# Performance work log

Hardware: AMD Instinct MI355X
Metric: run time of the kernel (lower is better)

The kernel has to match this reference:

```python
import jax, jax.numpy as jnp
import numpy as np

D_MODEL = 256
N_HEADS_SA = 8
CA_HEADS = 8
CA_DH = 64
CA_INNER = CA_HEADS * CA_DH  # 512
N_POINTS = 4
D_FFN = 1024
OFFSET_SCALE = 2.0
B, NQ = 4, 1024
T, H, W = 4, 64, 64
LV = T * H * W

PNAMES = ['sa_Wq','sa_bq','sa_Wk','sa_bk','sa_Wv','sa_bv','sa_Wo','sa_bo',
          'ln1_g','ln1_b','ln2_g','ln2_b','ln3_g','ln3_b',
          'ca_Wq','ca_bq','ca_Wk','ca_bk','ca_Wv','ca_bv','ca_Wref','ca_bref',
          'ca_Woff','ca_boff','ca_Wo','ca_bo',
          'ffn_W1','ffn_b1','ffn_W2','ffn_b2']


def _layer_norm(x, g, b, eps=1e-5):
    m = x.mean(-1, keepdims=True)
    v = ((x - m) ** 2).mean(-1, keepdims=True)
    return (x - m) * jax.lax.rsqrt(v + eps) * g + b


def _mha(q, k, v, Wq, bq, Wk, bk, Wv, bv, Wo, bo, n_heads):
    Bq, N, D = q.shape
    dh = D // n_heads
    scale = 1.0 / float(np.sqrt(dh))
    qh = (q @ Wq + bq).reshape(Bq, N, n_heads, dh)
    kh = (k @ Wk + bk).reshape(Bq, N, n_heads, dh)
    vh = (v @ Wv + bv).reshape(Bq, N, n_heads, dh)
    attn = jax.nn.softmax(jnp.einsum('bqhd,bkhd->bhqk', qh, kh) * scale, -1)
    out = jnp.einsum('bhqk,bkhd->bqhd', attn, vh).reshape(Bq, N, D)
    return out @ Wo + bo


def _trilinear_sample(vol, loc, sizes_f):
    # vol: [B, L, Hd, dh] flattened (T*H*W) volume per head
    # loc: [B, N, Hd, P, 3] normalized (t, h, w) coords in [0, 1]
    Bv, L, Hd, dh = vol.shape
    _, N, _, P, _ = loc.shape
    pos = jnp.clip(loc, 0.0, 1.0) * (sizes_f - 1.0)  # align_corners voxel coords
    p0 = jnp.floor(pos)
    frac = pos - p0
    p0i = p0.astype(jnp.int32)
    sizes_i = sizes_f.astype(jnp.int32)
    Hn, Wn = sizes_i[1], sizes_i[2]
    vol_t = vol.transpose(0, 2, 1, 3)  # [B, Hd, L, dh]
    out = jnp.zeros((Bv, Hd, N * P, dh), vol.dtype)
    for dt in (0, 1):
        for dy in (0, 1):
            for dx in (0, 1):
                c = jnp.minimum(p0i + jnp.array([dt, dy, dx], jnp.int32), sizes_i - 1)
                wt = (frac[..., 0] if dt else 1.0 - frac[..., 0]) \
                   * (frac[..., 1] if dy else 1.0 - frac[..., 1]) \
                   * (frac[..., 2] if dx else 1.0 - frac[..., 2])  # [B,N,Hd,P]
                idx = c[..., 0] * (Hn * Wn) + c[..., 1] * Wn + c[..., 2]
                idx_t = idx.transpose(0, 2, 1, 3).reshape(Bv, Hd, N * P, 1)
                g = jnp.take_along_axis(vol_t, idx_t, axis=2)  # [B,Hd,N*P,dh]
                w_t = wt.transpose(0, 2, 1, 3).reshape(Bv, Hd, N * P, 1)
                out = out + g * w_t
    return out.reshape(Bv, Hd, N, P, dh).transpose(0, 2, 1, 3, 4)  # [B,N,Hd,P,dh]


def _deform_cross_attn(query, key, value, flow_key, flow_value, spatial_shapes, p):
    Bq, N, _ = query.shape
    L = key.shape[1]
    sizes_f = spatial_shapes[0].astype(jnp.float32)  # single level (T, H, W)
    qh = (query @ p['ca_Wq'] + p['ca_bq']).reshape(Bq, N, CA_HEADS, CA_DH)
    ref = jax.nn.sigmoid(query @ p['ca_Wref'] + p['ca_bref'])  # [B,N,3]
    off = (query @ p['ca_Woff'] + p['ca_boff']).reshape(Bq, N, CA_HEADS, N_POINTS, 3)
    loc = ref[:, :, None, None, :] + off * (OFFSET_SCALE / sizes_f)
    k_vol = (key @ p['ca_Wk'] + p['ca_bk']).reshape(Bq, L, CA_HEADS, CA_DH)
    v_vol = (value @ p['ca_Wv'] + p['ca_bv']).reshape(Bq, L, CA_HEADS, CA_DH)
    fk_vol = (flow_key @ p['ca_Wk'] + p['ca_bk']).reshape(Bq, L, CA_HEADS, CA_DH)
    fv_vol = (flow_value @ p['ca_Wv'] + p['ca_bv']).reshape(Bq, L, CA_HEADS, CA_DH)
    k_s = _trilinear_sample(k_vol, loc, sizes_f)
    v_s = _trilinear_sample(v_vol, loc, sizes_f)
    fk_s = _trilinear_sample(fk_vol, loc, sizes_f)
    fv_s = _trilinear_sample(fv_vol, loc, sizes_f)
    scale = 1.0 / float(np.sqrt(CA_DH))
    logits = jnp.concatenate([
        jnp.einsum('bnhd,bnhpd->bnhp', qh, k_s),
        jnp.einsum('bnhd,bnhpd->bnhp', qh, fk_s)], -1) * scale
    attn = jax.nn.softmax(logits, -1)  # joint softmax over image+flow sampled points
    vals = jnp.concatenate([v_s, fv_s], 3)  # [B,N,Hd,2P,dh]
    out = jnp.einsum('bnhp,bnhpd->bnhd', attn, vals).reshape(Bq, N, CA_INNER)
    return out @ p['ca_Wo'] + p['ca_bo']


def _forward(query, query_pos, img, flow, pos_emb, spatial_shapes, p):
    q = query + query_pos
    sa = _mha(q, q, query, p['sa_Wq'], p['sa_bq'], p['sa_Wk'], p['sa_bk'],
              p['sa_Wv'], p['sa_bv'], p['sa_Wo'], p['sa_bo'], N_HEADS_SA)
    x = _layer_norm(query + sa, p['ln1_g'], p['ln1_b'])
    key = pos_emb + img
    flow_key = pos_emb + flow
    ca = _deform_cross_attn(x, key, img, flow_key, flow, spatial_shapes, p)
    x = _layer_norm(x + ca, p['ln2_g'], p['ln2_b'])
    ffn = jax.nn.relu(x @ p['ffn_W1'] + p['ffn_b1']) @ p['ffn_W2'] + p['ffn_b2']
    return _layer_norm(x + ffn, p['ln3_g'], p['ln3_b'])


def setup_inputs() -> dict:
    key = jax.random.key(0)
    ks = iter(jax.random.split(key, 64))
    def rn(shape, s=1.0):
        return jax.random.normal(next(ks), shape, jnp.float32) * s
    inp = {
        'query': rn((B, NQ, D_MODEL)),
        'query_pos': rn((B, NQ, D_MODEL)),
        'img_embed_flatten': rn((B, LV, D_MODEL)),
        'flow_embed_flatten': rn((B, LV, D_MODEL)),
        'indicator_temporal_lvl_pos_embed_flatten': rn((B, LV, D_MODEL)),
        'spatial_shapes': jnp.array([[T, H, W]], jnp.int32),
    }
    for nm in ['sa_Wq', 'sa_Wk', 'sa_Wv', 'sa_Wo']:
        inp[nm] = rn((D_MODEL, D_MODEL), 0.02)
    for nm in ['sa_bq', 'sa_bk', 'sa_bv', 'sa_bo', 'ln1_b', 'ln2_b', 'ln3_b']:
        inp[nm] = jnp.zeros((D_MODEL,), jnp.float32)
    for nm in ['ln1_g', 'ln2_g', 'ln3_g']:
        inp[nm] = jnp.ones((D_MODEL,), jnp.float32)
    inp['ca_Wq'] = rn((D_MODEL, CA_INNER), 0.02); inp['ca_bq'] = jnp.zeros((CA_INNER,), jnp.float32)
    inp['ca_Wk'] = rn((D_MODEL, CA_INNER), 0.02); inp['ca_bk'] = jnp.zeros((CA_INNER,), jnp.float32)
    inp['ca_Wv'] = rn((D_MODEL, CA_INNER), 0.02); inp['ca_bv'] = jnp.zeros((CA_INNER,), jnp.float32)
    inp['ca_Wref'] = rn((D_MODEL, 3), 0.02); inp['ca_bref'] = jnp.zeros((3,), jnp.float32)
    inp['ca_Woff'] = rn((D_MODEL, CA_HEADS * N_POINTS * 3), 0.02)
    inp['ca_boff'] = jnp.zeros((CA_HEADS * N_POINTS * 3,), jnp.float32)
    inp['ca_Wo'] = rn((CA_INNER, D_MODEL), 0.02); inp['ca_bo'] = jnp.zeros((D_MODEL,), jnp.float32)
    inp['ffn_W1'] = rn((D_MODEL, D_FFN), 0.02); inp['ffn_b1'] = jnp.zeros((D_FFN,), jnp.float32)
    inp['ffn_W2'] = rn((D_FFN, D_MODEL), 0.02); inp['ffn_b2'] = jnp.zeros((D_MODEL,), jnp.float32)
    return inp


def reference(query, query_pos, img_embed_flatten, flow_embed_flatten,
              indicator_temporal_lvl_pos_embed_flatten, spatial_shapes,
              sa_Wq, sa_bq, sa_Wk, sa_bk, sa_Wv, sa_bv, sa_Wo, sa_bo,
              ln1_g, ln1_b, ln2_g, ln2_b, ln3_g, ln3_b,
              ca_Wq, ca_bq, ca_Wk, ca_bk, ca_Wv, ca_bv, ca_Wref, ca_bref,
              ca_Woff, ca_boff, ca_Wo, ca_bo,
              ffn_W1, ffn_b1, ffn_W2, ffn_b2):
    p = dict(zip(PNAMES, (sa_Wq, sa_bq, sa_Wk, sa_bk, sa_Wv, sa_bv, sa_Wo, sa_bo,
                          ln1_g, ln1_b, ln2_g, ln2_b, ln3_g, ln3_b,
                          ca_Wq, ca_bq, ca_Wk, ca_bk, ca_Wv, ca_bv, ca_Wref, ca_bref,
                          ca_Woff, ca_boff, ca_Wo, ca_bo,
                          ffn_W1, ffn_b1, ffn_W2, ffn_b2)))
    return _forward(query, query_pos, img_embed_flatten, flow_embed_flatten,
                    indicator_temporal_lvl_pos_embed_flatten, spatial_shapes, p)
```

## Files before the change

### kernel.cpp

```cpp
#include <hip/hip_runtime.h>
#include <hip/hip_bf16.h>

#define BQ 4
#define NQT 1024
#define DM 256
#define HSA 8
#define DHSA 32
#define CAH 8
#define CADH 64
#define CAI 512
#define NPT 4
#define DFFN 1024
#define TT 4
#define HH 64
#define WW 64
#define LVOL 16384

using bf16 = __hip_bfloat16;
typedef __attribute__((ext_vector_type(4))) float fx4;
typedef __attribute__((ext_vector_type(8))) short s8v;
typedef __attribute__((ext_vector_type(4))) short s4v;

__device__ __forceinline__ float b2f(bf16 v) { return __bfloat162float(v); }
__device__ __forceinline__ bf16  f2b(float v) { return __float2bfloat16(v); }
__device__ __forceinline__ short f2bs(float v) {
  bf16 b = __float2bfloat16(v);
  return *reinterpret_cast<short*>(&b);
}

__device__ __forceinline__ float wave_sum64(float v) {
#pragma unroll
  for (int o = 32; o >= 1; o >>= 1) v += __shfl_xor(v, o, 64);
  return v;
}

__device__ __forceinline__ s8v pack8(float4 a, float4 b) {
  return (s8v){f2bs(a.x), f2bs(a.y), f2bs(a.z), f2bs(a.w),
               f2bs(b.x), f2bs(b.y), f2bs(b.z), f2bs(b.w)};
}

__device__ __forceinline__ void gl_lds16(const void* g, void* l) {
  __builtin_amdgcn_global_load_lds(
      (const __attribute__((address_space(1))) unsigned int*)g,
      (__attribute__((address_space(3))) unsigned int*)l, 16, 0, 0);
}

template <int KSH>
__global__ __launch_bounds__(256) void wtrans_k(const float* __restrict__ W,
                                               short* __restrict__ Wt, int N) {
  const int i = blockIdx.x * 256 + threadIdx.x;
  const int k = i & ((1 << KSH) - 1);
  const int n = i >> KSH;
  Wt[i] = f2bs(W[(size_t)k * N + n]);
}

template <int DUAL>
__global__ __launch_bounds__(256) void prep_k(const float* __restrict__ A,
                                              const float* __restrict__ B,
                                              short* __restrict__ O, int n4) {
  const int stride = gridDim.x * 256;
  for (int i = blockIdx.x * 256 + threadIdx.x; i < n4; i += stride) {
    float4 a = ((const float4*)A)[i];
    if (DUAL) {
      const float4 b = ((const float4*)B)[i];
      a.x += b.x; a.y += b.y; a.z += b.z; a.w += b.w;
    }
    ((s4v*)O)[i] = (s4v){f2bs(a.x), f2bs(a.y), f2bs(a.z), f2bs(a.w)};
  }
}

__global__ __launch_bounds__(256) void bgemm_k(
    const short* __restrict__ A, const short* __restrict__ Wt,
    const float* __restrict__ bias, bf16* __restrict__ Cout,
    int M, int N, int K) {
  __shared__ short As[2][128 * 32];
  __shared__ short Bs[2][128 * 32];
  const int tid = threadIdx.x;
  const int lane = tid & 63, w = tid >> 6;
  const int wr = w >> 1, wc = w & 1;
  const int lm = lane & 15, quad = lane >> 4;
  const int nwg = gridDim.x * gridDim.y;
  const int ib = blockIdx.y * gridDim.x + blockIdx.x;
  const int id = (ib & 7) * (nwg >> 3) + (ib >> 3);
  const int m0 = (id / gridDim.x) * 128;
  const int n0 = (id % gridDim.x) * 128;

  const int srow = lane >> 2;
  const int scol = (lane & 3) * 8;
  const size_t arow = (size_t)(m0 + w * 32 + srow);
  const size_t brow = (size_t)(n0 + w * 32 + srow);

  fx4 acc[4][4] = {};
  const int nt = K / 32;
  int cur = 0;
  {
    gl_lds16(&A[arow * K + scol], &As[0][(w * 32) * 32]);
    gl_lds16(&A[(arow + 16) * K + scol], &As[0][(w * 32 + 16) * 32]);
    gl_lds16(&Wt[brow * K + scol], &Bs[0][(w * 32) * 32]);
    gl_lds16(&Wt[(brow + 16) * K + scol], &Bs[0][(w * 32 + 16) * 32]);
  }
  __syncthreads();
  for (int t = 0; t < nt; t++) {
    if (t + 1 < nt) {
      const int k0 = (t + 1) * 32;
      gl_lds16(&A[arow * K + k0 + scol], &As[cur ^ 1][(w * 32) * 32]);
      gl_lds16(&A[(arow + 16) * K + k0 + scol], &As[cur ^ 1][(w * 32 + 16) * 32]);
      gl_lds16(&Wt[brow * K + k0 + scol], &Bs[cur ^ 1][(w * 32) * 32]);
      gl_lds16(&Wt[(brow + 16) * K + k0 + scol], &Bs[cur ^ 1][(w * 32 + 16) * 32]);
    }
    s8v af[4], bfr[4];
#pragma unroll
    for (int f = 0; f < 4; f++) {
      af[f] = *(s8v*)&As[cur][(wr * 64 + f * 16 + lm) * 32 + quad * 8];
      bfr[f] = *(s8v*)&Bs[cur][(wc * 64 + f * 16 + lm) * 32 + quad * 8];
    }
#pragma unroll
    for (int fm = 0; fm < 4; fm++)
#pragma unroll
      for (int fn = 0; fn < 4; fn++)
        acc[fm][fn] = __builtin_amdgcn_mfma_f32_16x16x32_bf16(
            af[fm], bfr[fn], acc[fm][fn], 0, 0, 0);
    __syncthreads();
    cur ^= 1;
  }
#pragma unroll
  for (int fn = 0; fn < 4; fn++) {
    const int n = n0 + wc * 64 + fn * 16 + lm;
    const float bb = bias[n];
#pragma unroll
    for (int fm = 0; fm < 4; fm++) {
      const int mbase = m0 + wr * 64 + fm * 16 + quad * 4;
#pragma unroll
      for (int r = 0; r < 4; r++)
        Cout[(size_t)(mbase + r) * N + n] = f2b(acc[fm][fn][r] + bb);
    }
  }
}

template <int DUAL, int RELU, int OUTBF>
__global__ __launch_bounds__(256) void mgemm_k(
    const float* __restrict__ A, const float* __restrict__ A2,
    const short* __restrict__ Wt, const float* __restrict__ bias,
    void* __restrict__ Cout, int M, int N, int K) {
  __shared__ short As[2][128 * 40];
  __shared__ short Bs[2][128 * 40];
  const int tid = threadIdx.x;
  const int lane = tid & 63, w = tid >> 6;
  const int wr = w >> 1, wc = w & 1;
  const int lm = lane & 15, quad = lane >> 4;
  const int nwg = gridDim.x * gridDim.y;
  const int ib = blockIdx.y * gridDim.x + blockIdx.x;
  const int id = (ib & 7) * (nwg >> 3) + (ib >> 3);
  const int m0 = (id / gridDim.x) * 128;
  const int n0 = (id % gridDim.x) * 128;

  const int am = tid >> 3, ak = (tid & 7) * 4;

  float4 pa[4], pa2[4];
  s8v pb[2];
  auto loadT = [&](int k0) {
#pragma unroll
    for (int i = 0; i < 4; i++) {
      pa[i] = *(const float4*)&A[(size_t)(m0 + am + i * 32) * K + k0 + ak];
      if (DUAL)
        pa2[i] = *(const float4*)&A2[(size_t)(m0 + am + i * 32) * K + k0 + ak];
    }
#pragma unroll
    for (int i = 0; i < 2; i++) {
      int unit = tid + i * 256;
      pb[i] = *(const s8v*)&Wt[(size_t)(n0 + (unit >> 2)) * K + k0 +
                               (unit & 3) * 8];
    }
  };
  auto stageT = [&](int buf) {
#pragma unroll
    for (int i = 0; i < 4; i++) {
      float x0 = pa[i].x, x1 = pa[i].y, x2 = pa[i].z, x3 = pa[i].w;
      if (DUAL) { x0 += pa2[i].x; x1 += pa2[i].y; x2 += pa2[i].z; x3 += pa2[i].w; }
      s4v sv = {f2bs(x0), f2bs(x1), f2bs(x2), f2bs(x3)};
      *(s4v*)&As[buf][(am + i * 32) * 40 + ak] = sv;
    }
#pragma unroll
    for (int i = 0; i < 2; i++) {
      int unit = tid + i * 256;
      *(s8v*)&Bs[buf][(unit >> 2) * 40 + (unit & 3) * 8] = pb[i];
    }
  };

  fx4 acc[4][4] = {};
  loadT(0);
  stageT(0);
  __syncthreads();
  int cur = 0;
  for (int k0 = 0; k0 < K; k0 += 32) {
    const int more = (k0 + 32 < K);
    if (more) loadT(k0 + 32);
    s8v af[4], bfr[4];
#pragma unroll
    for (int f = 0; f < 4; f++) {
      af[f] = *(s8v*)&As[cur][(wr * 64 + f * 16 + lm) * 40 + quad * 8];
      bfr[f] = *(s8v*)&Bs[cur][(wc * 64 + f * 16 + lm) * 40 + quad * 8];
    }
#pragma unroll
    for (int fm = 0; fm < 4; fm++)
#pragma unroll
      for (int fn = 0; fn < 4; fn++)
        acc[fm][fn] = __builtin_amdgcn_mfma_f32_16x16x32_bf16(
            af[fm], bfr[fn], acc[fm][fn], 0, 0, 0);
    if (more) stageT(cur ^ 1);
    __syncthreads();
    cur ^= 1;
  }
#pragma unroll
  for (int fn = 0; fn < 4; fn++) {
    const int n = n0 + wc * 64 + fn * 16 + lm;
    const float bb = bias[n];
#pragma unroll
    for (int fm = 0; fm < 4; fm++) {
      const int mbase = m0 + wr * 64 + fm * 16 + quad * 4;
#pragma unroll
      for (int r = 0; r < 4; r++) {
        float v = acc[fm][fn][r] + bb;
        if (RELU) v = fmaxf(v, 0.0f);
        const size_t off = (size_t)(mbase + r) * N + n;
        if (OUTBF)
          ((bf16*)Cout)[off] = f2b(v);
        else
          ((float*)Cout)[off] = v;
      }
    }
  }
}

__global__ __launch_bounds__(256) void sa_flash_k(
    const float* __restrict__ qh, const float* __restrict__ kh,
    const float* __restrict__ vh, float* __restrict__ op0,
    float* __restrict__ op1, float* __restrict__ mlb) {
  __shared__ short Ks[64 * 72];
  __shared__ short Vt[32 * 72];
  __shared__ short Ps[64 * 72];
  const int qt = blockIdx.x, h = blockIdx.y;
  const int b = blockIdx.z >> 1, half = blockIdx.z & 1;
  const int tid = threadIdx.x;
  const int w = tid >> 6, lane = tid & 63;
  const int lm = lane & 15, quad = lane >> 4;
  const size_t rowbase = (size_t)(b * NQT) * DM + h * DHSA;
  float* __restrict__ opart = half ? op1 : op0;
  float* __restrict__ ml = mlb + (size_t)half * (32768 * 2);

  s8v aq;
  {
    const int qrow = qt * 64 + w * 16 + lm;
    const float* qp = &qh[rowbase + (size_t)qrow * DM + quad * 8];
    const float4 q0 = *(const float4*)qp;
    const float4 q1 = *(const float4*)(qp + 4);
    const float sc = 0.17677669529663687f;
    aq = (s8v){f2bs(q0.x * sc), f2bs(q0.y * sc), f2bs(q0.z * sc), f2bs(q0.w * sc),
               f2bs(q1.x * sc), f2bs(q1.y * sc), f2bs(q1.z * sc), f2bs(q1.w * sc)};
  }

  fx4 o0 = {}, o1 = {};
  float mrun[4] = {-1e30f, -1e30f, -1e30f, -1e30f};
  float lrun[4] = {0.f, 0.f, 0.f, 0.f};
  const int jr = tid >> 2;
  const int d0 = (tid & 3) * 8;

  for (int jt = half * 8; jt < half * 8 + 8; jt++) {
    __syncthreads();
    {
      const size_t rb = rowbase + (size_t)(jt * 64 + jr) * DM + d0;
      const float4 k0 = *(const float4*)&kh[rb];
      const float4 k1 = *(const float4*)&kh[rb + 4];
      *(s8v*)&Ks[jr * 72 + d0] = pack8(k0, k1);
      const float4 v0 = *(const float4*)&vh[rb];
      const float4 v1 = *(const float4*)&vh[rb + 4];
      Vt[(d0 + 0) * 72 + jr] = f2bs(v0.x);
      Vt[(d0 + 1) * 72 + jr] = f2bs(v0.y);
      Vt[(d0 + 2) * 72 + jr] = f2bs(v0.z);
      Vt[(d0 + 3) * 72 + jr] = f2bs(v0.w);
      Vt[(d0 + 4) * 72 + jr] = f2bs(v1.x);
      Vt[(d0 + 5) * 72 + jr] = f2bs(v1.y);
      Vt[(d0 + 6) * 72 + jr] = f2bs(v1.z);
      Vt[(d0 + 7) * 72 + jr] = f2bs(v1.w);
    }
    __syncthreads();
    fx4 s[4];
    const fx4 zero = {};
#pragma unroll
    for (int nf = 0; nf < 4; nf++) {
      s8v kb = *(const s8v*)&Ks[(nf * 16 + lm) * 72 + quad * 8];
      s[nf] = __builtin_amdgcn_mfma_f32_16x16x32_bf16(aq, kb, zero, 0, 0, 0);
    }
#pragma unroll
    for (int r = 0; r < 4; r++) {
      float mx = fmaxf(fmaxf(s[0][r], s[1][r]), fmaxf(s[2][r], s[3][r]));
#pragma unroll
      for (int off = 8; off >= 1; off >>= 1)
        mx = fmaxf(mx, __shfl_xor(mx, off, 64));
      const float mnew = fmaxf(mrun[r], mx);
      const float corr = expf(mrun[r] - mnew);
      mrun[r] = mnew;
      float p0 = expf(s[0][r] - mnew);
      float p1 = expf(s[1][r] - mnew);
      float p2 = expf(s[2][r] - mnew);
      float p3 = expf(s[3][r] - mnew);
      float rs = p0 + p1 + p2 + p3;
#pragma unroll
      for (int off = 8; off >= 1; off >>= 1) rs += __shfl_xor(rs, off, 64);
      lrun[r] = lrun[r] * corr + rs;
      o0[r] *= corr;
      o1[r] *= corr;
      s[0][r] = p0; s[1][r] = p1; s[2][r] = p2; s[3][r] = p3;
    }
#pragma unroll
    for (int nf = 0; nf < 4; nf++)
#pragma unroll
      for (int r = 0; r < 4; r++)
        Ps[(w * 16 + quad * 4 + r) * 72 + nf * 16 + lm] = f2bs(s[nf][r]);
#pragma unroll
    for (int ks = 0; ks < 2; ks++) {
      s8v pf = *(const s8v*)&Ps[(w * 16 + lm) * 72 + ks * 32 + quad * 8];
      s8v vb0 = *(const s8v*)&Vt[lm * 72 + ks * 32 + quad * 8];
      s8v vb1 = *(const s8v*)&Vt[(16 + lm) * 72 + ks * 32 + quad * 8];
      o0 = __builtin_amdgcn_mfma_f32_16x16x32_bf16(pf, vb0, o0, 0, 0, 0);
      o1 = __builtin_amdgcn_mfma_f32_16x16x32_bf16(pf, vb1, o1, 0, 0, 0);
    }
  }
#pragma unroll
  for (int r = 0; r < 4; r++) {
    const int row = qt * 64 + w * 16 + quad * 4 + r;
    const size_t base = rowbase + (size_t)row * DM;
    opart[base + lm] = o0[r];
    opart[base + 16 + lm] = o1[r];
    if (lm == 0) {
      const int rowid = (b * 8 + h) * 1024 + row;
      ml[(size_t)rowid * 2] = mrun[r];
      ml[(size_t)rowid * 2 + 1] = lrun[r];
    }
  }
}

__global__ __launch_bounds__(256) void sa_merge_k(
    const float* __restrict__ op0, const float* __restrict__ op1,
    const float* __restrict__ mlb, float* __restrict__ outp) {
  const int t = blockIdx.x * 256 + threadIdx.x;
  const int d = t & 31;
  const int rowid = t >> 5;
  const int n = rowid & 1023, h = (rowid >> 10) & 7, b = rowid >> 13;
  const size_t addr = ((size_t)(b * NQT + n)) * DM + h * DHSA + d;
  const float m0 = mlb[(size_t)rowid * 2], l0 = mlb[(size_t)rowid * 2 + 1];
  const float m1 = mlb[65536 + (size_t)rowid * 2];
  const float l1 = mlb[65536 + (size_t)rowid * 2 + 1];
  const float M = fmaxf(m0, m1);
  const float w0 = expf(m0 - M), w1 = expf(m1 - M);
  const float inv = 1.0f / (l0 * w0 + l1 * w1);
  outp[addr] = (op0[addr] * w0 + op1[addr] * w1) * inv;
}

__global__ __launch_bounds__(128) void refoff_k(
    const float* __restrict__ x1, const float* __restrict__ Wref,
    const float* __restrict__ bref, const float* __restrict__ Woff,
    const float* __restrict__ boff, float* __restrict__ refb,
    float* __restrict__ offb) {
  __shared__ float xs[256];
  const int row = blockIdx.x;
  const int tid = threadIdx.x;
  xs[tid] = x1[(size_t)row * DM + tid];
  xs[tid + 128] = x1[(size_t)row * DM + tid + 128];
  __syncthreads();
  if (tid < 3) {
    float s = bref[tid];
    for (int d = 0; d < 256; d++) s = fmaf(xs[d], Wref[d * 3 + tid], s);
    refb[(size_t)row * 3 + tid] = 1.0f / (1.0f + expf(-s));
  } else if (tid < 99) {
    int o = tid - 3;
    float s = boff[o];
    for (int d = 0; d < 256; d++) s = fmaf(xs[d], Woff[d * 96 + o], s);
    offb[(size_t)row * 96 + o] = s;
  }
}

__device__ __forceinline__ void calc_corners(
    const float* __restrict__ refb, const float* __restrict__ offb, int bn,
    int h, int (&idxs)[NPT][8], float (&wts)[NPT][8]) {
  const float rt = refb[bn * 3 + 0], ry = refb[bn * 3 + 1], rx = refb[bn * 3 + 2];
  const float* ofp = &offb[(size_t)bn * 96 + h * 12];
#pragma unroll
  for (int p = 0; p < NPT; p++) {
    float lt = rt + ofp[p * 3 + 0] * 0.5f;
    float ly = ry + ofp[p * 3 + 1] * 0.03125f;
    float lx = rx + ofp[p * 3 + 2] * 0.03125f;
    float pt = fminf(fmaxf(lt, 0.f), 1.f) * (TT - 1);
    float py = fminf(fmaxf(ly, 0.f), 1.f) * (HH - 1);
    float px = fminf(fmaxf(lx, 0.f), 1.f) * (WW - 1);
    float f0t = floorf(pt), f0y = floorf(py), f0x = floorf(px);
    float frt = pt - f0t, fry = py - f0y, frx = px - f0x;
    int t0 = (int)f0t, y0 = (int)f0y, x0 = (int)f0x;
    int t1 = min(t0 + 1, TT - 1), y1 = min(y0 + 1, HH - 1), x1 = min(x0 + 1, WW - 1);
    float wt0 = 1.f - frt, wy0 = 1.f - fry, wx0 = 1.f - frx;
#pragma unroll
    for (int c = 0; c < 8; c++) {
      int dt = c >> 2, dy = (c >> 1) & 1, dx = c & 1;
      int ct = dt ? t1 : t0, cy = dy ? y1 : y0, cx = dx ? x1 : x0;
      idxs[p][c] = ct * (HH * WW) + cy * WW + cx;
      wts[p][c] = (dt ? frt : wt0) * (dy ? fry : wy0) * (dx ? frx : wx0);
    }
  }
}

__global__ __launch_bounds__(256) void ca_logits_k(
    const float* __restrict__ qh, const float* __restrict__ refb,
    const float* __restrict__ offb, const bf16* __restrict__ vol,
    float* __restrict__ logits, int slot) {
  const int wid = (blockIdx.x * blockDim.x + threadIdx.x) >> 6;
  const int lane = threadIdx.x & 63;
  const int h = wid & 7;
  const int bn = wid >> 3;
  const int b = bn >> 10;
  const float q = qh[(size_t)bn * CAI + h * CADH + lane];
  int idxs[NPT][8];
  float wts[NPT][8];
  calc_corners(refb, offb, bn, h, idxs, wts);
  const size_t volbase = (size_t)b * LVOL * CAI + h * CADH + lane;
  float* lp = logits + ((size_t)bn * CAH + h) * 8 + slot;
#pragma unroll
  for (int p = 0; p < NPT; p++) {
    float ks = 0.f;
#pragma unroll
    for (int c = 0; c < 8; c++)
      ks = fmaf(wts[p][c], b2f(vol[volbase + (size_t)idxs[p][c] * CAI]), ks);
    float li = wave_sum64(q * ks) * 0.125f;
    if (lane == p) lp[p] = li;
  }
}

__global__ __launch_bounds__(256) void ca_softmax_k(float* __restrict__ logits) {
  const int i = blockIdx.x * blockDim.x + threadIdx.x;
  float* p = logits + (size_t)i * 8;
  float v[8], m = -1e30f;
#pragma unroll
  for (int j = 0; j < 8; j++) { v[j] = p[j]; m = fmaxf(m, v[j]); }
  float s = 0.f;
#pragma unroll
  for (int j = 0; j < 8; j++) { v[j] = expf(v[j] - m); s += v[j]; }
  const float inv = 1.0f / s;
#pragma unroll
  for (int j = 0; j < 8; j++) p[j] = v[j] * inv;
}

template <int FIRST>
__global__ __launch_bounds__(256) void ca_acc_k(
    const float* __restrict__ refb, const float* __restrict__ offb,
    const bf16* __restrict__ vol, const float* __restrict__ attn,
    float* __restrict__ acc, int slot) {
  const int wid = (blockIdx.x * blockDim.x + threadIdx.x) >> 6;
  const int lane = threadIdx.x & 63;
  const int h = wid & 7;
  const int bn = wid >> 3;
  const int b = bn >> 10;
  int idxs[NPT][8];
  float wts[NPT][8];
  calc_corners(refb, offb, bn, h, idxs, wts);
  const size_t volbase = (size_t)b * LVOL * CAI + h * CADH + lane;
  const float* ap = attn + ((size_t)bn * CAH + h) * 8 + slot;
  const size_t off = (size_t)bn * CAI + h * CADH + lane;
  float a = FIRST ? 0.f : acc[off];
#pragma unroll
  for (int p = 0; p < NPT; p++) {
    float vs = 0.f;
#pragma unroll
    for (int c = 0; c < 8; c++)
      vs = fmaf(wts[p][c], b2f(vol[volbase + (size_t)idxs[p][c] * CAI]), vs);
    a = fmaf(ap[p], vs, a);
  }
  acc[off] = a;
}

__global__ __launch_bounds__(256) void ln_k(
    const float* __restrict__ resv, const float* __restrict__ x,
    const float* __restrict__ g, const float* __restrict__ bb,
    float* __restrict__ of) {
  const int row = (blockIdx.x * blockDim.x + threadIdx.x) >> 6;
  const int lane = threadIdx.x & 63;
  const size_t base = (size_t)row * DM;
  float v[4];
#pragma unroll
  for (int i = 0; i < 4; i++) {
    int d = lane + i * 64;
    v[i] = resv[base + d] + x[base + d];
  }
  float s = wave_sum64(v[0] + v[1] + v[2] + v[3]);
  const float mean = s * (1.0f / 256.0f);
  float vs = 0.f;
#pragma unroll
  for (int i = 0; i < 4; i++) { float d0 = v[i] - mean; vs = fmaf(d0, d0, vs); }
  vs = wave_sum64(vs);
  const float rstd = rsqrtf(vs * (1.0f / 256.0f) + 1e-5f);
#pragma unroll
  for (int i = 0; i < 4; i++) {
    int d = lane + i * 64;
    of[base + d] = (v[i] - mean) * rstd * g[d] + bb[d];
  }
}

extern "C" void kernel_launch(void* const* d_in, const int* in_sizes, int n_in,
                              void* d_out, int out_size, void* d_ws,
                              size_t ws_size, hipStream_t stream) {
  const float* query = (const float*)d_in[0];
  const float* qpos = (const float*)d_in[1];
  const float* img = (const float*)d_in[2];
  const float* flow = (const float*)d_in[3];
  const float* pos = (const float*)d_in[4];
  const float* sa_Wq = (const float*)d_in[6];
  const float* sa_Wk = (const float*)d_in[7];
  const float* sa_Wv = (const float*)d_in[8];
  const float* sa_Wo = (const float*)d_in[9];
  const float* sa_bq = (const float*)d_in[10];
  const float* sa_bk = (const float*)d_in[11];
  const float* sa_bv = (const float*)d_in[12];
  const float* sa_bo = (const float*)d_in[13];
  const float* ln1_b = (const float*)d_in[14];
  const float* ln2_b = (const float*)d_in[15];
  const float* ln3_b = (const float*)d_in[16];
  const float* ln1_g = (const float*)d_in[17];
  const float* ln2_g = (const float*)d_in[18];
  const float* ln3_g = (const float*)d_in[19];
  const float* ca_Wq = (const float*)d_in[20];
  const float* ca_bq = (const float*)d_in[21];
  const float* ca_Wk = (const float*)d_in[22];
  const float* ca_bk = (const float*)d_in[23];
  const float* ca_Wv = (const float*)d_in[24];
  const float* ca_bv = (const float*)d_in[25];
  const float* ca_Wref = (const float*)d_in[26];
  const float* ca_bref = (const float*)d_in[27];
  const float* ca_Woff = (const float*)d_in[28];
  const float* ca_boff = (const float*)d_in[29];
  const float* ca_Wo = (const float*)d_in[30];
  const float* ca_bo = (const float*)d_in[31];
  const float* ffn_W1 = (const float*)d_in[32];
  const float* ffn_b1 = (const float*)d_in[33];
  const float* ffn_W2 = (const float*)d_in[34];
  const float* ffn_b2 = (const float*)d_in[35];

  const int MQ = BQ * NQT;
  const int MV = BQ * LVOL;
  const size_t MB = 1024 * 1024;

  char* r0 = (char*)d_ws;
  char* w = r0 + 64 * MB;
  auto alloc = [&](size_t n) {
    char* p = w;
    w += (n + 255) & ~(size_t)255;
    return p;
  };
  float* x1_f = (float*)alloc((size_t)MQ * DM * 4);
  float* ca_qh = (float*)alloc((size_t)MQ * CAI * 4);
  float* refb = (float*)alloc((size_t)MQ * 3 * 4);
  float* offb = (float*)alloc((size_t)MQ * 96 * 4);
  float* logits = (float*)alloc((size_t)MQ * CAH * 8 * 4);
  float* ca_acc = (float*)alloc((size_t)MQ * CAI * 4);
  short* WtsaQ = (short*)alloc((size_t)DM * DM * 2);
  short* WtsaK = (short*)alloc((size_t)DM * DM * 2);
  short* WtsaV = (short*)alloc((size_t)DM * DM * 2);
  short* WtsaO = (short*)alloc((size_t)DM * DM * 2);
  short* Wtcaq = (short*)alloc((size_t)CAI * DM * 2);
  short* Wtk = (short*)alloc((size_t)CAI * DM * 2);
  short* Wtv = (short*)alloc((size_t)CAI * DM * 2);
  short* Wtcao = (short*)alloc((size_t)DM * CAI * 2);
  short* Wtf1 = (short*)alloc((size_t)DFFN * DM * 2);
  short* Wtf2 = (short*)alloc((size_t)DM * DFFN * 2);
  short* abuf = (short*)alloc((size_t)MV * DM * 2);
  if ((size_t)(w - (char*)d_ws) > ws_size) return;

  float* qh_sa = (float*)(r0 + 0 * MB);
  float* kh_sa = (float*)(r0 + 4 * MB);
  float* vh_sa = (float*)(r0 + 8 * MB);
  float* sa_att = (float*)(r0 + 12 * MB);
  float* sa_proj = (float*)(r0 + 16 * MB);
  float* o_p0 = (float*)(r0 + 20 * MB);
  float* o_p1 = (float*)(r0 + 24 * MB);
  float* mlb = (float*)(r0 + 28 * MB);
  bf16* vol = (bf16*)r0;
  float* ca_o = (float*)(r0 + 0 * MB);
  float* x2_f = (float*)(r0 + 4 * MB);
  float* ffn_h = (float*)(r0 + 8 * MB);
  float* ffn_o = (float*)(r0 + 24 * MB);

  const int n4v = MV * DM / 4;

  dim3 blk(256);
  wtrans_k<8><<<dim3(DM * DM / 256), blk, 0, stream>>>(sa_Wq, WtsaQ, DM);
  wtrans_k<8><<<dim3(DM * DM / 256), blk, 0, stream>>>(sa_Wk, WtsaK, DM);
  wtrans_k<8><<<dim3(DM * DM / 256), blk, 0, stream>>>(sa_Wv, WtsaV, DM);
  wtrans_k<8><<<dim3(DM * DM / 256), blk, 0, stream>>>(sa_Wo, WtsaO, DM);
  wtrans_k<8><<<dim3(DM * CAI / 256), blk, 0, stream>>>(ca_Wq, Wtcaq, CAI);
  wtrans_k<8><<<dim3(DM * CAI / 256), blk, 0, stream>>>(ca_Wk, Wtk, CAI);
  wtrans_k<8><<<dim3(DM * CAI / 256), blk, 0, stream>>>(ca_Wv, Wtv, CAI);
  wtrans_k<8><<<dim3(DM * DFFN / 256), blk, 0, stream>>>(ffn_W1, Wtf1, DFFN);
  wtrans_k<9><<<dim3(CAI * DM / 256), blk, 0, stream>>>(ca_Wo, Wtcao, DM);
  wtrans_k<10><<<dim3(DFFN * DM / 256), blk, 0, stream>>>(ffn_W2, Wtf2, DM);
  mgemm_k<1, 0, 0><<<dim3(DM / 128, MQ / 128), blk, 0, stream>>>(query, qpos, WtsaQ, sa_bq, (void*)qh_sa, MQ, DM, DM);
  mgemm_k<1, 0, 0><<<dim3(DM / 128, MQ / 128), blk, 0, stream>>>(query, qpos, WtsaK, sa_bk, (void*)kh_sa, MQ, DM, DM);
  mgemm_k<0, 0, 0><<<dim3(DM / 128, MQ / 128), blk, 0, stream>>>(query, query, WtsaV, sa_bv, (void*)vh_sa, MQ, DM, DM);
  sa_flash_k<<<dim3(16, 8, 8), blk, 0, stream>>>(qh_sa, kh_sa, vh_sa, o_p0, o_p1, mlb);
  sa_merge_k<<<dim3(4096), blk, 0, stream>>>(o_p0, o_p1, mlb, sa_att);
  mgemm_k<0, 0, 0><<<dim3(DM / 128, MQ / 128), blk, 0, stream>>>(sa_att, sa_att, WtsaO, sa_bo, (void*)sa_proj, MQ, DM, DM);
  ln_k<<<dim3(MQ / 4), blk, 0, stream>>>(query, sa_proj, ln1_g, ln1_b, x1_f);
  mgemm_k<0, 0, 0><<<dim3(CAI / 128, MQ / 128), blk, 0, stream>>>(x1_f, x1_f, Wtcaq, ca_bq, (void*)ca_qh, MQ, CAI, DM);
  refoff_k<<<dim3(MQ), dim3(128), 0, stream>>>(x1_f, ca_Wref, ca_bref, ca_Woff, ca_boff, refb, offb);
  prep_k<1><<<dim3(2048), blk, 0, stream>>>(pos, img, abuf, n4v);
  bgemm_k<<<dim3(CAI / 128, MV / 128), blk, 0, stream>>>(abuf, Wtk, ca_bk, vol, MV, CAI, DM);
  ca_logits_k<<<dim3(8192), blk, 0, stream>>>(ca_qh, refb, offb, vol, logits, 0);
  prep_k<1><<<dim3(2048), blk, 0, stream>>>(pos, flow, abuf, n4v);
  bgemm_k<<<dim3(CAI / 128, MV / 128), blk, 0, stream>>>(abuf, Wtk, ca_bk, vol, MV, CAI, DM);
  ca_logits_k<<<dim3(8192), blk, 0, stream>>>(ca_qh, refb, offb, vol, logits, 4);
  ca_softmax_k<<<dim3(128), blk, 0, stream>>>(logits);
  prep_k<0><<<dim3(2048), blk, 0, stream>>>(img, img, abuf, n4v);
  bgemm_k<<<dim3(CAI / 128, MV / 128), blk, 0, stream>>>(abuf, Wtv, ca_bv, vol, MV, CAI, DM);
  ca_acc_k<1><<<dim3(8192), blk, 0, stream>>>(refb, offb, vol, logits, ca_acc, 0);
  prep_k<0><<<dim3(2048), blk, 0, stream>>>(flow, flow, abuf, n4v);
  bgemm_k<<<dim3(CAI / 128, MV / 128), blk, 0, stream>>>(abuf, Wtv, ca_bv, vol, MV, CAI, DM);
  ca_acc_k<0><<<dim3(8192), blk, 0, stream>>>(refb, offb, vol, logits, ca_acc, 4);
  mgemm_k<0, 0, 0><<<dim3(DM / 128, MQ / 128), blk, 0, stream>>>(ca_acc, ca_acc, Wtcao, ca_bo, (void*)ca_o, MQ, DM, CAI);
  ln_k<<<dim3(MQ / 4), blk, 0, stream>>>(x1_f, ca_o, ln2_g, ln2_b, x2_f);
  mgemm_k<0, 1, 0><<<dim3(DFFN / 128, MQ / 128), blk, 0, stream>>>(x2_f, x2_f, Wtf1, ffn_b1, (void*)ffn_h, MQ, DFFN, DM);
  mgemm_k<0, 0, 0><<<dim3(DM / 128, MQ / 128), blk, 0, stream>>>(ffn_h, ffn_h, Wtf2, ffn_b2, (void*)ffn_o, MQ, DM, DFFN);
  ln_k<<<dim3(MQ / 4), blk, 0, stream>>>(x2_f, ffn_o, ln3_g, ln3_b, (float*)d_out);
}
```

Measured before the change: 728.5 us.

## Fuse fp32-to-bf16 prep into volume GEMMs, batch weight transposes, use 64-tile GEMMs

The separate prep kernels that summed or converted the fp32 volume inputs into a bf16 staging buffer are removed. The volume GEMM now loads fp32 A tiles into registers, adds and converts them, and stores them to LDS, which saves a full write and read of the 16K x 256 staging buffer for each of four passes. The ten weight-transpose launches are merged into one kernel, and the small query-side GEMMs switch to a 64x64 tile kernel so they launch more workgroups. The cost is register-staged A loads in place of direct global-to-LDS loads, plus smaller tiles with less reuse per block.

```diff
diff --git a/kernel.cpp b/kernel.cpp
--- a/kernel.cpp
+++ b/kernel.cpp
@@ -45,35 +45,30 @@
       (__attribute__((address_space(3))) unsigned int*)l, 16, 0, 0);
 }
 
-template <int KSH>
-__global__ __launch_bounds__(256) void wtrans_k(const float* __restrict__ W,
-                                               short* __restrict__ Wt, int N) {
-  const int i = blockIdx.x * 256 + threadIdx.x;
-  const int k = i & ((1 << KSH) - 1);
-  const int n = i >> KSH;
-  Wt[i] = f2bs(W[(size_t)k * N + n]);
+struct WtransArgs {
+  const float* W[10];
+  short* Wt[10];
+};
+__global__ __launch_bounds__(256) void wtrans_all_k(WtransArgs a) {
+  const int blk = blockIdx.x;
+  int seg, start, ksh, N;
+  if (blk < 1024)      { seg = blk >> 8; start = seg << 8; ksh = 8; N = 256; }
+  else if (blk < 2560) { seg = 4 + ((blk - 1024) >> 9); start = 1024 + ((seg - 4) << 9); ksh = 8; N = 512; }
+  else if (blk < 3584) { seg = 7; start = 2560; ksh = 8; N = 1024; }
+  else if (blk < 4096) { seg = 8; start = 3584; ksh = 9; N = 256; }
+  else                 { seg = 9; start = 4096; ksh = 10; N = 256; }
+  const int i = (blk - start) * 256 + threadIdx.x;
+  const int k = i & ((1 << ksh) - 1);
+  const int n = i >> ksh;
+  a.Wt[seg][i] = f2bs(a.W[seg][(size_t)k * N + n]);
 }
 
 template <int DUAL>
-__global__ __launch_bounds__(256) void prep_k(const float* __restrict__ A,
-                                              const float* __restrict__ B,
-                                              short* __restrict__ O, int n4) {
-  const int stride = gridDim.x * 256;
-  for (int i = blockIdx.x * 256 + threadIdx.x; i < n4; i += stride) {
-    float4 a = ((const float4*)A)[i];
-    if (DUAL) {
-      const float4 b = ((const float4*)B)[i];
-      a.x += b.x; a.y += b.y; a.z += b.z; a.w += b.w;
-    }
-    ((s4v*)O)[i] = (s4v){f2bs(a.x), f2bs(a.y), f2bs(a.z), f2bs(a.w)};
-  }
-}
-
-__global__ __launch_bounds__(256) void bgemm_k(
-    const short* __restrict__ A, const short* __restrict__ Wt,
-    const float* __restrict__ bias, bf16* __restrict__ Cout,
-    int M, int N, int K) {
-  __shared__ short As[2][128 * 32];
+__global__ __launch_bounds__(256) void vgemm_k(
+    const float* __restrict__ A, const float* __restrict__ A2,
+    const short* __restrict__ Wt, const float* __restrict__ bias,
+    bf16* __restrict__ Cout, int M, int N, int K) {
+  __shared__ short As[2][128 * 40];
   __shared__ short Bs[2][128 * 32];
   const int tid = threadIdx.x;
   const int lane = tid & 63, w = tid >> 6;
@@ -85,33 +80,49 @@
   const int m0 = (id / gridDim.x) * 128;
   const int n0 = (id % gridDim.x) * 128;
 
-  const int srow = lane >> 2;
-  const int scol = (lane & 3) * 8;
-  const size_t arow = (size_t)(m0 + w * 32 + srow);
-  const size_t brow = (size_t)(n0 + w * 32 + srow);
+  const int am = tid >> 3, ak = (tid & 7) * 4;
+  const size_t brow = (size_t)(n0 + w * 32 + (lane >> 2));
+  const int bcol = (lane & 3) * 8;
+
+  float4 pa[4], pa2[4];
+  auto loadA = [&](int k0) {
+#pragma unroll
+    for (int i = 0; i < 4; i++) {
+      pa[i] = *(const float4*)&A[(size_t)(m0 + am + i * 32) * K + k0 + ak];
+      if (DUAL)
+        pa2[i] = *(const float4*)&A2[(size_t)(m0 + am + i * 32) * K + k0 + ak];
+    }
+  };
+  auto glB = [&](int k0, int buf) {
+    gl_lds16(&Wt[brow * K + k0 + bcol], &Bs[buf][(w * 32) * 32]);
+    gl_lds16(&Wt[(brow + 16) * K + k0 + bcol], &Bs[buf][(w * 32 + 16) * 32]);
+  };
+  auto stageA = [&](int buf) {
+#pragma unroll
+    for (int i = 0; i < 4; i++) {
+      float x0 = pa[i].x, x1 = pa[i].y, x2 = pa[i].z, x3 = pa[i].w;
+      if (DUAL) { x0 += pa2[i].x; x1 += pa2[i].y; x2 += pa2[i].z; x3 += pa2[i].w; }
+      *(s4v*)&As[buf][(am + i * 32) * 40 + ak] =
+          (s4v){f2bs(x0), f2bs(x1), f2bs(x2), f2bs(x3)};
+    }
+  };
 
   fx4 acc[4][4] = {};
-  const int nt = K / 32;
+  loadA(0);
+  glB(0, 0);
+  stageA(0);
+  __syncthreads();
   int cur = 0;
-  {
-    gl_lds16(&A[arow * K + scol], &As[0][(w * 32) * 32]);
-    gl_lds16(&A[(arow + 16) * K + scol], &As[0][(w * 32 + 16) * 32]);
-    gl_lds16(&Wt[brow * K + scol], &Bs[0][(w * 32) * 32]);
-    gl_lds16(&Wt[(brow + 16) * K + scol], &Bs[0][(w * 32 + 16) * 32]);
-  }
-  __syncthreads();
-  for (int t = 0; t < nt; t++) {
-    if (t + 1 < nt) {
-      const int k0 = (t + 1) * 32;
-      gl_lds16(&A[arow * K + k0 + scol], &As[cur ^ 1][(w * 32) * 32]);
-      gl_lds16(&A[(arow + 16) * K + k0 + scol], &As[cur ^ 1][(w * 32 + 16) * 32]);
-      gl_lds16(&Wt[brow * K + k0 + scol], &Bs[cur ^ 1][(w * 32) * 32]);
-      gl_lds16(&Wt[(brow + 16) * K + k0 + scol], &Bs[cur ^ 1][(w * 32 + 16) * 32]);
+  for (int k0 = 0; k0 < K; k0 += 32) {
+    const int more = (k0 + 32 < K);
+    if (more) {
+      loadA(k0 + 32);
+      glB(k0 + 32, cur ^ 1);
     }
     s8v af[4], bfr[4];
 #pragma unroll
     for (int f = 0; f < 4; f++) {
-      af[f] = *(s8v*)&As[cur][(wr * 64 + f * 16 + lm) * 32 + quad * 8];
+      af[f] = *(s8v*)&As[cur][(wr * 64 + f * 16 + lm) * 40 + quad * 8];
       bfr[f] = *(s8v*)&Bs[cur][(wc * 64 + f * 16 + lm) * 32 + quad * 8];
     }
 #pragma unroll
@@ -120,6 +131,7 @@
       for (int fn = 0; fn < 4; fn++)
         acc[fm][fn] = __builtin_amdgcn_mfma_f32_16x16x32_bf16(
             af[fm], bfr[fn], acc[fm][fn], 0, 0, 0);
+    if (more) stageA(cur ^ 1);
     __syncthreads();
     cur ^= 1;
   }
@@ -133,6 +145,86 @@
 #pragma unroll
       for (int r = 0; r < 4; r++)
         Cout[(size_t)(mbase + r) * N + n] = f2b(acc[fm][fn][r] + bb);
+    }
+  }
+}
+
+template <int DUAL>
+__global__ __launch_bounds__(256) void mgemm64_k(
+    const float* __restrict__ A, const float* __restrict__ A2,
+    const short* __restrict__ Wt, const float* __restrict__ bias,
+    float* __restrict__ Cout, int M, int N, int K) {
+  __shared__ short As[2][64 * 40];
+  __shared__ short Bs[2][64 * 40];
+  const int tid = threadIdx.x;
+  const int lane = tid & 63, w = tid >> 6;
+  const int wr = w >> 1, wc = w & 1;
+  const int lm = lane & 15, quad = lane >> 4;
+  const int nwg = gridDim.x * gridDim.y;
+  const int ib = blockIdx.y * gridDim.x + blockIdx.x;
+  const int id = (ib & 7) * (nwg >> 3) + (ib >> 3);
+  const int m0 = (id / gridDim.x) * 64;
+  const int n0 = (id % gridDim.x) * 64;
+
+  const int am = tid >> 2, ak = (tid & 3) * 8;
+  const int bn = tid >> 2, bc = (tid & 3) * 8;
+
+  float4 pa0, pa1, qa0, qa1;
+  s8v pb;
+  auto loadT = [&](int k0) {
+    pa0 = *(const float4*)&A[(size_t)(m0 + am) * K + k0 + ak];
+    pa1 = *(const float4*)&A[(size_t)(m0 + am) * K + k0 + ak + 4];
+    if (DUAL) {
+      qa0 = *(const float4*)&A2[(size_t)(m0 + am) * K + k0 + ak];
+      qa1 = *(const float4*)&A2[(size_t)(m0 + am) * K + k0 + ak + 4];
+    }
+    pb = *(const s8v*)&Wt[(size_t)(n0 + bn) * K + k0 + bc];
+  };
+  auto stageT = [&](int buf) {
+    float4 u = pa0, v = pa1;
+    if (DUAL) {
+      u.x += qa0.x; u.y += qa0.y; u.z += qa0.z; u.w += qa0.w;
+      v.x += qa1.x; v.y += qa1.y; v.z += qa1.z; v.w += qa1.w;
+    }
+    *(s4v*)&As[buf][am * 40 + ak] = (s4v){f2bs(u.x), f2bs(u.y), f2bs(u.z), f2bs(u.w)};
+    *(s4v*)&As[buf][am * 40 + ak + 4] = (s4v){f2bs(v.x), f2bs(v.y), f2bs(v.z), f2bs(v.w)};
+    *(s8v*)&Bs[buf][bn * 40 + bc] = pb;
+  };
+
+  fx4 acc[2][2] = {};
+  loadT(0);
+  stageT(0);
+  __syncthreads();
+  int cur = 0;
+  for (int k0 = 0; k0 < K; k0 += 32) {
+    const int more = (k0 + 32 < K);
+    if (more) loadT(k0 + 32);
+    s8v af[2], bfr[2];
+#pragma unroll
+    for (int f = 0; f < 2; f++) {
+      af[f] = *(s8v*)&As[cur][(wr * 32 + f * 16 + lm) * 40 + quad * 8];
+      bfr[f] = *(s8v*)&Bs[cur][(wc * 32 + f * 16 + lm) * 40 + quad * 8];
+    }
+#pragma unroll
+    for (int fm = 0; fm < 2; fm++)
+#pragma unroll
+      for (int fn = 0; fn < 2; fn++)
+        acc[fm][fn] = __builtin_amdgcn_mfma_f32_16x16x32_bf16(
+            af[fm], bfr[fn], acc[fm][fn], 0, 0, 0);
+    if (more) stageT(cur ^ 1);
+    __syncthreads();
+    cur ^= 1;
+  }
+#pragma unroll
+  for (int fn = 0; fn < 2; fn++) {
+    const int n = n0 + wc * 32 + fn * 16 + lm;
+    const float bb = bias[n];
+#pragma unroll
+    for (int fm = 0; fm < 2; fm++) {
+      const int mbase = m0 + wr * 32 + fm * 16 + quad * 4;
+#pragma unroll
+      for (int r = 0; r < 4; r++)
+        Cout[(size_t)(mbase + r) * N + n] = acc[fm][fn][r] + bb;
     }
   }
 }
@@ -569,7 +661,6 @@
   short* Wtcao = (short*)alloc((size_t)DM * CAI * 2);
   short* Wtf1 = (short*)alloc((size_t)DFFN * DM * 2);
   short* Wtf2 = (short*)alloc((size_t)DM * DFFN * 2);
-  short* abuf = (short*)alloc((size_t)MV * DM * 2);
   if ((size_t)(w - (char*)d_ws) > ws_size) return;
 
   float* qh_sa = (float*)(r0 + 0 * MB);
@@ -586,44 +677,40 @@
   float* ffn_h = (float*)(r0 + 8 * MB);
   float* ffn_o = (float*)(r0 + 24 * MB);
 
-  const int n4v = MV * DM / 4;
-
   dim3 blk(256);
-  wtrans_k<8><<<dim3(DM * DM / 256), blk, 0, stream>>>(sa_Wq, WtsaQ, DM);
-  wtrans_k<8><<<dim3(DM * DM / 256), blk, 0, stream>>>(sa_Wk, WtsaK, DM);
-  wtrans_k<8><<<dim3(DM * DM / 256), blk, 0, stream>>>(sa_Wv, WtsaV, DM);
-  wtrans_k<8><<<dim3(DM * DM / 256), blk, 0, stream>>>(sa_Wo, WtsaO, DM);
-  wtrans_k<8><<<dim3(DM * CAI / 256), blk, 0, stream>>>(ca_Wq, Wtcaq, CAI);
-  wtrans_k<8><<<dim3(DM * CAI / 256), blk, 0, stream>>>(ca_Wk, Wtk, CAI);
-  wtrans_k<8><<<dim3(DM * CAI / 256), blk, 0, stream>>>(ca_Wv, Wtv, CAI);
-  wtrans_k<8><<<dim3(DM * DFFN / 256), blk, 0, stream>>>(ffn_W1, Wtf1, DFFN);
-  wtrans_k<9><<<dim3(CAI * DM / 256), blk, 0, stream>>>(ca_Wo, Wtcao, DM);
-  wtrans_k<10><<<dim3(DFFN * DM / 256), blk, 0, stream>>>(ffn_W2, Wtf2, DM);
-  mgemm_k<1, 0, 0><<<dim3(DM / 128, MQ / 128), blk, 0, stream>>>(query, qpos, WtsaQ, sa_bq, (void*)qh_sa, MQ, DM, DM);
-  mgemm_k<1, 0, 0><<<dim3(DM / 128, MQ / 128), blk, 0, stream>>>(query, qpos, WtsaK, sa_bk, (void*)kh_sa, MQ, DM, DM);
-  mgemm_k<0, 0, 0><<<dim3(DM / 128, MQ / 128), blk, 0, stream>>>(query, query, WtsaV, sa_bv, (void*)vh_sa, MQ, DM, DM);
+  WtransArgs wa;
+  wa.W[0] = sa_Wq;  wa.Wt[0] = WtsaQ;
+  wa.W[1] = sa_Wk;  wa.Wt[1] = WtsaK;
+  wa.W[2] = sa_Wv;  wa.Wt[2] = WtsaV;
+  wa.W[3] = sa_Wo;  wa.Wt[3] = WtsaO;
+  wa.W[4] = ca_Wq;  wa.Wt[4] = Wtcaq;
+  wa.W[5] = ca_Wk;  wa.Wt[5] = Wtk;
+  wa.W[6] = ca_Wv;  wa.Wt[6] = Wtv;
+  wa.W[7] = ffn_W1; wa.Wt[7] = Wtf1;
+  wa.W[8] = ca_Wo;  wa.Wt[8] = Wtcao;
+  wa.W[9] = ffn_W2; wa.Wt[9] = Wtf2;
+  wtrans_all_k<<<dim3(5120), blk, 0, stream>>>(wa);
+  mgemm64_k<1><<<dim3(DM / 64, MQ / 64), blk, 0, stream>>>(query, qpos, WtsaQ, sa_bq, qh_sa, MQ, DM, DM);
+  mgemm64_k<1><<<dim3(DM / 64, MQ / 64), blk, 0, stream>>>(query, qpos, WtsaK, sa_bk, kh_sa, MQ, DM, DM);
+  mgemm64_k<0><<<dim3(DM / 64, MQ / 64), blk, 0, stream>>>(query, query, WtsaV, sa_bv, vh_sa, MQ, DM, DM);
   sa_flash_k<<<dim3(16, 8, 8), blk, 0, stream>>>(qh_sa, kh_sa, vh_sa, o_p0, o_p1, mlb);
   sa_merge_k<<<dim3(4096), blk, 0, stream>>>(o_p0, o_p1, mlb, sa_att);
-  mgemm_k<0, 0, 0><<<dim3(DM / 128, MQ / 128), blk, 0, stream>>>(sa_att, sa_att, WtsaO, sa_bo, (void*)sa_proj, MQ, DM, DM);
+  mgemm64_k<0><<<dim3(DM / 64, MQ / 64), blk, 0, stream>>>(sa_att, sa_att, WtsaO, sa_bo, sa_proj, MQ, DM, DM);
   ln_k<<<dim3(MQ / 4), blk, 0, stream>>>(query, sa_proj, ln1_g, ln1_b, x1_f);
-  mgemm_k<0, 0, 0><<<dim3(CAI / 128, MQ / 128), blk, 0, stream>>>(x1_f, x1_f, Wtcaq, ca_bq, (void*)ca_qh, MQ, CAI, DM);
+  mgemm64_k<0><<<dim3(CAI / 64, MQ / 64), blk, 0, stream>>>(x1_f, x1_f, Wtcaq, ca_bq, ca_qh, MQ, CAI, DM);
   refoff_k<<<dim3(MQ), dim3(128), 0, stream>>>(x1_f, ca_Wref, ca_bref, ca_Woff, ca_boff, refb, offb);
-  prep_k<1><<<dim3(2048), blk, 0, stream>>>(pos, img, abuf, n4v);
-  bgemm_k<<<dim3(CAI / 128, MV / 128), blk, 0, stream>>>(abuf, Wtk, ca_bk, vol, MV, CAI, DM);
+  vgemm_k<1><<<dim3(CAI / 128, MV / 128), blk, 0, stream>>>(pos, img, Wtk, ca_bk, vol, MV, CAI, DM);
   ca_logits_k<<<dim3(8192), blk, 0, stream>>>(ca_qh, refb, offb, vol, logits, 0);
-  prep_k<1><<<dim3(2048), blk, 0, stream>>>(pos, flow, abuf, n4v);
-  bgemm_k<<<dim3(CAI / 128, MV / 128), blk, 0, stream>>>(abuf, Wtk, ca_bk, vol, MV, CAI, DM);
+  vgemm_k<1><<<dim3(CAI / 128, MV / 128), blk, 0, stream>>>(pos, flow, Wtk, ca_bk, vol, MV, CAI, DM);
   ca_logits_k<<<dim3(8192), blk, 0, stream>>>(ca_qh, refb, offb, vol, logits, 4);
   ca_softmax_k<<<dim3(128), blk, 0, stream>>>(logits);
-  prep_k<0><<<dim3(2048), blk, 0, stream>>>(img, img, abuf, n4v);
-  bgemm_k<<<dim3(CAI / 128, MV / 128), blk, 0, stream>>>(abuf, Wtv, ca_bv, vol, MV, CAI, DM);
+  vgemm_k<0><<<dim3(CAI / 128, MV / 128), blk, 0, stream>>>(img, img, Wtv, ca_bv, vol, MV, CAI, DM);
   ca_acc_k<1><<<dim3(8192), blk, 0, stream>>>(refb, offb, vol, logits, ca_acc, 0);
-  prep_k<0><<<dim3(2048), blk, 0, stream>>>(flow, flow, abuf, n4v);
-  bgemm_k<<<dim3(CAI / 128, MV / 128), blk, 0, stream>>>(abuf, Wtv, ca_bv, vol, MV, CAI, DM);
+  vgemm_k<0><<<dim3(CAI / 128, MV / 128), blk, 0, stream>>>(flow, flow, Wtv, ca_bv, vol, MV, CAI, DM);
   ca_acc_k<0><<<dim3(8192), blk, 0, stream>>>(refb, offb, vol, logits, ca_acc, 4);
-  mgemm_k<0, 0, 0><<<dim3(DM / 128, MQ / 128), blk, 0, stream>>>(ca_acc, ca_acc, Wtcao, ca_bo, (void*)ca_o, MQ, DM, CAI);
+  mgemm64_k<0><<<dim3(DM / 64, MQ / 64), blk, 0, stream>>>(ca_acc, ca_acc, Wtcao, ca_bo, ca_o, MQ, DM, CAI);
   ln_k<<<dim3(MQ / 4), blk, 0, stream>>>(x1_f, ca_o, ln2_g, ln2_b, x2_f);
   mgemm_k<0, 1, 0><<<dim3(DFFN / 128, MQ / 128), blk, 0, stream>>>(x2_f, x2_f, Wtf1, ffn_b1, (void*)ffn_h, MQ, DFFN, DM);
-  mgemm_k<0, 0, 0><<<dim3(DM / 128, MQ / 128), blk, 0, stream>>>(ffn_h, ffn_h, Wtf2, ffn_b2, (void*)ffn_o, MQ, DM, DFFN);
+  mgemm64_k<0><<<dim3(DM / 64, MQ / 64), blk, 0, stream>>>(ffn_h, ffn_h, Wtf2, ffn_b2, ffn_o, MQ, DM, DFFN);
   ln_k<<<dim3(MQ / 4), blk, 0, stream>>>(x2_f, ffn_o, ln3_g, ln3_b, (float*)d_out);
 }
```

New measurement: 698.6 us. 4.1% less time.
